# Performance work log

Hardware: AMD Instinct MI355X
Metric: run time of the kernel (lower is better)

## Reference

```python
import jax, jax.numpy as jnp
import numpy as np

N_NODES = 100000
N_EDGES = 1600000
IN_CH = 128
HEADS = 4
HID = 32
OUT_CH = 128
NEG_SLOPE = 0.2


def setup_inputs() -> dict:
    key = jax.random.key(0)
    ks = jax.random.split(key, 7)
    sc = 1.0 / np.sqrt(IN_CH)
    return {
        "x": jax.random.normal(ks[0], (N_NODES, IN_CH), dtype=jnp.float32),
        "edge_index": jax.random.randint(ks[1], (2, N_EDGES), 0, N_NODES, dtype=jnp.int32),
        "W": jax.random.normal(ks[2], (IN_CH, HEADS * HID), dtype=jnp.float32) * sc,
        "att_src": jax.random.normal(ks[3], (HEADS, HID), dtype=jnp.float32) * sc,
        "att_dst": jax.random.normal(ks[4], (HEADS, HID), dtype=jnp.float32) * sc,
        "lin_w": jax.random.normal(ks[5], (HEADS * HID, OUT_CH), dtype=jnp.float32) * (1.0 / np.sqrt(HEADS * HID)),
        "lin_b": jax.random.normal(ks[6], (OUT_CH,), dtype=jnp.float32) * 0.01,
    }


def reference(x, edge_index, W, att_src, att_dst, lin_w, lin_b):
    N = x.shape[0]
    src, dst = edge_index[0], edge_index[1]
    # node-wise linear transform -> [N, H, C]
    h = (x @ W).reshape(N, HEADS, HID)
    # per-node attention logit components [N, H]
    a_src = jnp.einsum("nhc,hc->nh", h, att_src)
    a_dst = jnp.einsum("nhc,hc->nh", h, att_dst)
    # per-edge logits with LeakyReLU [E, H]
    e = jax.nn.leaky_relu(a_src[src] + a_dst[dst], negative_slope=NEG_SLOPE)
    # segment softmax over destination neighborhoods
    m = jax.ops.segment_max(e, dst, num_segments=N)
    ex = jnp.exp(e - m[dst])
    s = jax.ops.segment_sum(ex, dst, num_segments=N)
    alpha = ex / (s[dst] + 1e-16)
    # weighted scatter-sum of source features [N, H, C] -> concat heads
    msg = h[src] * alpha[:, :, None]
    out = jax.ops.segment_sum(msg, dst, num_segments=N).reshape(N, HEADS * HID)
    # trailing dense + ReLU
    return jax.nn.relu(out @ lin_w + lin_b)
```

## Files before the change

### kernel.cpp

```cpp
#include <hip/hip_runtime.h>
#include <hip/hip_fp16.h>

#define NB    256
#define BSH   9
#define HBLK  384
#define BBLK  512

typedef _Float16 f16;
typedef _Float16 half8 __attribute__((ext_vector_type(8)));
typedef __fp16 pk16x2 __attribute__((ext_vector_type(2)));
typedef float f32x4 __attribute__((ext_vector_type(4)));

__global__ __launch_bounds__(256) void k_setup(
    const float* __restrict__ W, const float* __restrict__ LW,
    f16* __restrict__ Wt, f16* __restrict__ LWt,
    const int* __restrict__ dst, int* __restrict__ btot, int E, int chunk)
{
    int b = blockIdx.x;
    int t = threadIdx.x;
    if (b < 128) {
        if (t < 128) Wt[b * 128 + t]           = (f16)W[t * 128 + b];
        else         LWt[b * 128 + (t - 128)]  = (f16)LW[(t - 128) * 128 + b];
        return;
    }
    __shared__ int h[NB];
    h[t] = 0;
    __syncthreads();
    int blk = b - 128;
    int e0 = blk * chunk;
    int e1 = min(e0 + chunk, E);
    for (int e = e0 + t; e < e1; e += 256)
        atomicAdd(&h[dst[e] >> BSH], 1);
    __syncthreads();
    if (h[t]) atomicAdd(&btot[t], h[t]);
}

__global__ __launch_bounds__(256) void k_gemm_att(
    const float* __restrict__ A, const f16* __restrict__ Wt,
    const float* __restrict__ att_s, const float* __restrict__ att_d,
    f16* __restrict__ Hh, float* __restrict__ as_out, float* __restrict__ ad_out,
    int M)
{
    __shared__ __align__(16) f16 as_lds[64 * 136];
    int t = threadIdx.x;
    int row0 = blockIdx.x * 64;

    {
        int r = t >> 2, kq = (t & 3) * 32;
        const float* ap = A + (size_t)(row0 + r) * 128 + kq;
        bool valid = (row0 + r) < M;
        pk16x2 hb[16];
#pragma unroll
        for (int j = 0; j < 8; ++j) {
            float4 v = valid ? *(const float4*)(ap + j * 4) : make_float4(0.f, 0.f, 0.f, 0.f);
            hb[2 * j]     = __builtin_amdgcn_cvt_pkrtz(v.x, v.y);
            hb[2 * j + 1] = __builtin_amdgcn_cvt_pkrtz(v.z, v.w);
        }
        f16* dst = as_lds + r * 136 + kq;
#pragma unroll
        for (int j = 0; j < 4; ++j) *(float4*)(dst + j * 8) = ((float4*)hb)[j];
    }
    __syncthreads();

    int w = t >> 6, ln = t & 63;
    int rr = (w & 1) * 32;
    int cc = (w >> 1) * 64;
    int q = ln >> 4, m = ln & 15;

    f32x4 acc[2][4];
#pragma unroll
    for (int i = 0; i < 2; ++i)
#pragma unroll
        for (int j = 0; j < 4; ++j) acc[i][j] = (f32x4){0.f, 0.f, 0.f, 0.f};

    const f16* wp = Wt + (size_t)(cc + m) * 128 + q * 8;
#pragma unroll
    for (int ks = 0; ks < 4; ++ks) {
        int k0 = ks * 32 + q * 8;
        half8 a0 = *(const half8*)(as_lds + (rr + m) * 136 + k0);
        half8 a1 = *(const half8*)(as_lds + (rr + 16 + m) * 136 + k0);
        half8 bf[4];
#pragma unroll
        for (int j = 0; j < 4; ++j)
            bf[j] = *(const half8*)(wp + j * 16 * 128 + ks * 32);
#pragma unroll
        for (int j = 0; j < 4; ++j) {
            acc[0][j] = __builtin_amdgcn_mfma_f32_16x16x32_f16(a0, bf[j], acc[0][j], 0, 0, 0);
            acc[1][j] = __builtin_amdgcn_mfma_f32_16x16x32_f16(a1, bf[j], acc[1][j], 0, 0, 0);
        }
    }
    __syncthreads();
#pragma unroll
    for (int i = 0; i < 2; ++i)
#pragma unroll
        for (int j = 0; j < 4; ++j)
#pragma unroll
            for (int g = 0; g < 4; ++g)
                as_lds[(rr + i * 16 + q * 4 + g) * 136 + cc + j * 16 + m] = (f16)acc[i][j][g];
    __syncthreads();
    {
        int r = t >> 2, cq = (t & 3) * 32;
        if (row0 + r < M) {
            float4 o0 = *(const float4*)(as_lds + r * 136 + cq);
            float4 o1 = *(const float4*)(as_lds + r * 136 + cq + 8);
            float4 o2 = *(const float4*)(as_lds + r * 136 + cq + 16);
            float4 o3 = *(const float4*)(as_lds + r * 136 + cq + 24);
            float4* hp = (float4*)(Hh + (size_t)(row0 + r) * 128 + cq);
            hp[0] = o0; hp[1] = o1; hp[2] = o2; hp[3] = o3;
        }
    }
    {
        int rl = w * 16 + m;
        int head = q;
        float ds = 0.f, dd = 0.f;
#pragma unroll
        for (int ch = 0; ch < 4; ++ch) {
            half8 hv = *(const half8*)(as_lds + rl * 136 + head * 32 + ch * 8);
            float4 s0 = *(const float4*)(att_s + head * 32 + ch * 8);
            float4 s1 = *(const float4*)(att_s + head * 32 + ch * 8 + 4);
            float4 d0 = *(const float4*)(att_d + head * 32 + ch * 8);
            float4 d1 = *(const float4*)(att_d + head * 32 + ch * 8 + 4);
            ds += (float)hv[0] * s0.x + (float)hv[1] * s0.y + (float)hv[2] * s0.z + (float)hv[3] * s0.w
                + (float)hv[4] * s1.x + (float)hv[5] * s1.y + (float)hv[6] * s1.z + (float)hv[7] * s1.w;
            dd += (float)hv[0] * d0.x + (float)hv[1] * d0.y + (float)hv[2] * d0.z + (float)hv[3] * d0.w
                + (float)hv[4] * d1.x + (float)hv[5] * d1.y + (float)hv[6] * d1.z + (float)hv[7] * d1.w;
        }
        if (row0 + rl < M) {
            as_out[(row0 + rl) * 4 + head] = ds;
            ad_out[(row0 + rl) * 4 + head] = dd;
        }
    }
}

__global__ __launch_bounds__(256) void k_bin(
    const int* __restrict__ ei, const int* __restrict__ btot,
    int* __restrict__ bres, int* __restrict__ binned, int E, int chunk)
{
    __shared__ int h[NB];
    __shared__ int base_s[NB];
    __shared__ int ws[4];
    int t = threadIdx.x;
    {
        int v = btot[t];
        int lane = t & 63, w = t >> 6;
        int x = v;
#pragma unroll
        for (int o = 1; o < 64; o <<= 1) {
            int y = __shfl_up(x, o);
            if (lane >= o) x += y;
        }
        if (lane == 63) ws[w] = x;
        __syncthreads();
        int wb = 0;
#pragma unroll
        for (int k = 0; k < 4; ++k) wb += (k < w) ? ws[k] : 0;
        base_s[t] = wb + x - v;
    }
    h[t] = 0;
    __syncthreads();
    int e0 = blockIdx.x * chunk;
    int e1 = min(e0 + chunk, E);
    for (int e = e0 + t; e < e1; e += 256)
        atomicAdd(&h[ei[E + e] >> BSH], 1);
    __syncthreads();
    int cnt = h[t];
    int mybase = base_s[t] + (cnt ? atomicAdd(&bres[t], cnt) : 0);
    __syncthreads();
    h[t] = mybase;
    __syncthreads();
    for (int e = e0 + t; e < e1; e += 256) {
        int s = ei[e];
        int d = ei[E + e];
        int p = atomicAdd(&h[d >> BSH], 1);
        binned[p] = s | ((d & ((1 << BSH) - 1)) << 17);
    }
}

__global__ __launch_bounds__(256) void k_ph_csr(
    const int* __restrict__ binned, const int* __restrict__ btot,
    int* __restrict__ csr, int* __restrict__ off, int* __restrict__ deg,
    int N, int E)
{
    __shared__ int cnt[512], loff[512], sd[256];
    __shared__ int base_s[NB];
    __shared__ int ws[4];
    int b = blockIdx.x;
    int lo = b << BSH;
    if (lo >= N) return;
    int t = threadIdx.x;
    {
        int v = btot[t];
        int lane = t & 63, w = t >> 6;
        int x = v;
#pragma unroll
        for (int o = 1; o < 64; o <<= 1) {
            int y = __shfl_up(x, o);
            if (lane >= o) x += y;
        }
        if (lane == 63) ws[w] = x;
        __syncthreads();
        int wb = 0;
#pragma unroll
        for (int k = 0; k < 4; ++k) wb += (k < w) ? ws[k] : 0;
        base_s[t] = wb + x - v;
    }
    cnt[t] = 0; cnt[t + 256] = 0;
    __syncthreads();
    int seg = base_s[b];
    int len = btot[b];
    for (int i = t; i < len; i += 256)
        atomicAdd(&cnt[(unsigned)binned[seg + i] >> 17], 1);
    __syncthreads();
    int a0 = cnt[2 * t], a1 = cnt[2 * t + 1];
    int s = a0 + a1;
    sd[t] = s;
    __syncthreads();
    for (int o = 1; o < 256; o <<= 1) {
        int x = (t >= o) ? sd[t - o] : 0;
        __syncthreads();
        sd[t] += x;
        __syncthreads();
    }
    int ex = sd[t] - s;
    loff[2 * t] = ex;
    loff[2 * t + 1] = ex + a0;
    int n0 = lo + 2 * t;
    if (n0 < N)     { off[n0] = seg + ex;          deg[n0] = a0; }
    if (n0 + 1 < N) { off[n0 + 1] = seg + ex + a0; deg[n0 + 1] = a1; }
    __syncthreads();
    for (int i = t; i < len; i += 256) {
        int v = binned[seg + i];
        int p = atomicAdd(&loff[(unsigned)v >> 17], 1);
        csr[seg + p] = v & 0x1ffff;
    }
}

__global__ __launch_bounds__(256) void k_gather_fused(
    const __half* __restrict__ Hh, const float* __restrict__ as_,
    const float* __restrict__ ad_, const int* __restrict__ off,
    const int* __restrict__ deg, const int* __restrict__ csr,
    const f16* __restrict__ LWt, const float* __restrict__ bias,
    float* __restrict__ Out, int N)
{
    __shared__ __align__(16) __half2 wh[16][68];
    __shared__ int srcs[16][16];
    __shared__ __align__(16) f16 pt[16][136];
    int t = threadIdx.x;
    int wid = t >> 6, lane = t & 63;
    int sub = lane >> 4;
    int li = lane & 15;
    int hh = li >> 2;
    int slot = wid * 4 + sub;
    int gbase = blockIdx.x * 16;
    int n = gbase + slot;
    bool nvalid = n < N;
    int dg = nvalid ? deg[n] : 0;
    int base = nvalid ? off[n] : 0;
    float4 adn = nvalid ? *(const float4*)(ad_ + (size_t)n * 4)
                        : make_float4(0.f, 0.f, 0.f, 0.f);

    float s0 = 0.f, s1 = 0.f, s2 = 0.f, s3 = 0.f;
    float acc[8] = {0.f, 0.f, 0.f, 0.f, 0.f, 0.f, 0.f, 0.f};

    for (int c0 = 0; c0 < dg; c0 += 16) {
        int cnt = min(16, dg - c0);
        {
            int idx = c0 + li;
            int se = csr[base + min(idx, dg - 1)];
            float4 as = *(const float4*)(as_ + (size_t)se * 4);
            float e0 = as.x + adn.x, e1 = as.y + adn.y;
            float e2 = as.z + adn.z, e3 = as.w + adn.w;
            e0 = fmaxf(e0, 0.2f * e0); e1 = fmaxf(e1, 0.2f * e1);
            e2 = fmaxf(e2, 0.2f * e2); e3 = fmaxf(e3, 0.2f * e3);
            float x0 = __expf(e0), x1 = __expf(e1);
            float x2 = __expf(e2), x3 = __expf(e3);
            if (idx >= dg) { x0 = x1 = x2 = x3 = 0.f; }
            s0 += x0; s1 += x1; s2 += x2; s3 += x3;
            __half2 w4[4];
            w4[0] = __float2half2_rn(x0);
            w4[1] = __float2half2_rn(x1);
            w4[2] = __float2half2_rn(x2);
            w4[3] = __float2half2_rn(x3);
            *(float4*)&wh[slot][li * 4] = *(float4*)w4;
            srcs[slot][li] = se;
        }
        __asm__ volatile("s_waitcnt lgkmcnt(0)" ::: "memory");
        int quads = (cnt + 3) >> 2;
        __half2 ah[4];
        ah[0] = ah[1] = ah[2] = ah[3] = __float2half2_rn(0.f);
        for (int qq = 0; qq < quads; ++qq) {
#pragma unroll
            for (int u = 0; u < 4; ++u) {
                int i = qq * 4 + u;
                __half2 w2 = wh[slot][i * 4 + hh];
                int se = srcs[slot][i];
                float4 raw = *(const float4*)(Hh + (size_t)se * 128 + li * 8);
                __half2* ph = (__half2*)&raw;
                ah[0] = __hfma2(ph[0], w2, ah[0]);
                ah[1] = __hfma2(ph[1], w2, ah[1]);
                ah[2] = __hfma2(ph[2], w2, ah[2]);
                ah[3] = __hfma2(ph[3], w2, ah[3]);
            }
            if ((qq & 1) == 1) {
#pragma unroll
                for (int k = 0; k < 4; ++k) {
                    float2 f = __half22float2(ah[k]);
                    acc[2 * k] += f.x; acc[2 * k + 1] += f.y;
                    ah[k] = __float2half2_rn(0.f);
                }
            }
        }
#pragma unroll
        for (int k = 0; k < 4; ++k) {
            float2 f = __half22float2(ah[k]);
            acc[2 * k] += f.x; acc[2 * k + 1] += f.y;
        }
        __asm__ volatile("s_waitcnt lgkmcnt(0)" ::: "memory");
    }

#pragma unroll
    for (int o = 1; o < 16; o <<= 1) {
        s0 += __shfl_xor(s0, o);
        s1 += __shfl_xor(s1, o);
        s2 += __shfl_xor(s2, o);
        s3 += __shfl_xor(s3, o);
    }
    float sh = (hh == 0) ? s0 : (hh == 1) ? s1 : (hh == 2) ? s2 : s3;
    float inv = 1.f / (sh + 1e-16f);
    {
        __half2 o4[4];
#pragma unroll
        for (int k = 0; k < 4; ++k)
            o4[k] = __float22half2_rn(make_float2(acc[2 * k] * inv, acc[2 * k + 1] * inv));
        *(float4*)&pt[slot][li * 8] = *(float4*)o4;
    }
    __syncthreads();

    {
        int cc = wid * 32;
        f32x4 acc2[2];
        acc2[0] = (f32x4){0.f, 0.f, 0.f, 0.f};
        acc2[1] = (f32x4){0.f, 0.f, 0.f, 0.f};
        const f16* wp = LWt + (size_t)(cc + li) * 128 + sub * 8;
#pragma unroll
        for (int ks = 0; ks < 4; ++ks) {
            half8 a0 = *(const half8*)&pt[li][ks * 32 + sub * 8];
            half8 b0 = *(const half8*)(wp + ks * 32);
            half8 b1 = *(const half8*)(wp + 16 * 128 + ks * 32);
            acc2[0] = __builtin_amdgcn_mfma_f32_16x16x32_f16(a0, b0, acc2[0], 0, 0, 0);
            acc2[1] = __builtin_amdgcn_mfma_f32_16x16x32_f16(a0, b1, acc2[1], 0, 0, 0);
        }
        float bv0 = bias[cc + li];
        float bv1 = bias[cc + 16 + li];
#pragma unroll
        for (int g = 0; g < 4; ++g) {
            int r = sub * 4 + g;
            int node = gbase + r;
            if (node < N) {
                Out[(size_t)node * 128 + cc + li]      = fmaxf(acc2[0][g] + bv0, 0.f);
                Out[(size_t)node * 128 + cc + 16 + li] = fmaxf(acc2[1][g] + bv1, 0.f);
            }
        }
    }
}


extern "C" void kernel_launch(void* const* d_in, const int* in_sizes, int n_in,
                              void* d_out, int out_size, void* d_ws, size_t ws_size,
                              hipStream_t stream)
{
    const float* x     = (const float*)d_in[0];
    const int*   ei    = (const int*)d_in[1];
    const float* W     = (const float*)d_in[2];
    const float* att_s = (const float*)d_in[3];
    const float* att_d = (const float*)d_in[4];
    const float* lin_w = (const float*)d_in[5];
    const float* lin_b = (const float*)d_in[6];
    float* out = (float*)d_out;
    int N = in_sizes[0] / 128;
    int E = in_sizes[1] / 2;

    char* p = (char*)d_ws;
    auto alloc = [&](size_t bytes) { char* r = p; p += (bytes + 255) & ~(size_t)255; return r; };
    f16*    Hh   = (f16*)alloc((size_t)N * 128 * 2);
    f16*    Wt   = (f16*)alloc(128 * 128 * 2);
    f16*    LWt  = (f16*)alloc(128 * 128 * 2);
    float*  AS   = (float*)alloc((size_t)N * 4 * 4);
    float*  AD   = (float*)alloc((size_t)N * 4 * 4);
    int*    deg  = (int*)alloc((size_t)N * 4);
    int*    off  = (int*)alloc((size_t)N * 4);
    int*    btot = (int*)alloc((size_t)NB * 4 * 2);
    int*    bres = btot + NB;
    int*    csr  = (int*)alloc((size_t)E * 4);
    int*    binned = (int*)alloc((size_t)E * 4);

    int hchunk = (E + HBLK - 1) / HBLK;
    int bchunk = (E + BBLK - 1) / BBLK;
    int mb = (N + 63) / 64;
    hipMemsetAsync(btot, 0, (size_t)NB * 4 * 2, stream);
    k_setup<<<128 + HBLK, 256, 0, stream>>>(W, lin_w, Wt, LWt, ei + E, btot, E, hchunk);
    k_gemm_att<<<mb, 256, 0, stream>>>(x, Wt, att_s, att_d, Hh, AS, AD, N);
    k_bin<<<BBLK, 256, 0, stream>>>(ei, btot, bres, binned, E, bchunk);
    k_ph_csr<<<NB, 256, 0, stream>>>(binned, btot, csr, off, deg, N, E);
    k_gather_fused<<<(N + 15) / 16, 256, 0, stream>>>(
        (const __half*)Hh, AS, AD, off, deg, csr, LWt, lin_b, out, N);
}
```

Baseline: 280.5 us.

## Double-buffer gather feature loads and halve CSR bin width

The gather loop now loads the next quad of source feature rows into a second register buffer while the current quad is accumulated, so global load latency overlaps with the half-precision FMAs. Separately, destination bins shrink from 512 to 256 nodes, giving 512 bins. The per-block full prefix scan in the CSR kernel is replaced by a reduction over the preceding bin totals. The cost is more registers for the double buffer and extra redundant loads at the tail, since indices are clamped to quad 0.

```diff
diff --git a/kernel.cpp b/kernel.cpp
--- a/kernel.cpp
+++ b/kernel.cpp
@@ -1,8 +1,8 @@
 #include <hip/hip_runtime.h>
 #include <hip/hip_fp16.h>
 
-#define NB    256
-#define BSH   9
+#define NB    512
+#define BSH   8
 #define HBLK  384
 #define BBLK  512
 
@@ -24,7 +24,7 @@
         return;
     }
     __shared__ int h[NB];
-    h[t] = 0;
+    h[t] = 0; h[t + 256] = 0;
     __syncthreads();
     int blk = b - 128;
     int e0 = blk * chunk;
@@ -32,7 +32,8 @@
     for (int e = e0 + t; e < e1; e += 256)
         atomicAdd(&h[dst[e] >> BSH], 1);
     __syncthreads();
-    if (h[t]) atomicAdd(&btot[t], h[t]);
+    if (h[t])       atomicAdd(&btot[t], h[t]);
+    if (h[t + 256]) atomicAdd(&btot[t + 256], h[t + 256]);
 }
 
 __global__ __launch_bounds__(256) void k_gemm_att(
@@ -141,9 +142,10 @@
     __shared__ int ws[4];
     int t = threadIdx.x;
     {
-        int v = btot[t];
+        int v0 = btot[2 * t], v1 = btot[2 * t + 1];
+        int s = v0 + v1;
         int lane = t & 63, w = t >> 6;
-        int x = v;
+        int x = s;
 #pragma unroll
         for (int o = 1; o < 64; o <<= 1) {
             int y = __shfl_up(x, o);
@@ -154,19 +156,22 @@
         int wb = 0;
 #pragma unroll
         for (int k = 0; k < 4; ++k) wb += (k < w) ? ws[k] : 0;
-        base_s[t] = wb + x - v;
-    }
-    h[t] = 0;
+        int ex = wb + x - s;
+        base_s[2 * t] = ex;
+        base_s[2 * t + 1] = ex + v0;
+    }
+    h[t] = 0; h[t + 256] = 0;
     __syncthreads();
     int e0 = blockIdx.x * chunk;
     int e1 = min(e0 + chunk, E);
     for (int e = e0 + t; e < e1; e += 256)
         atomicAdd(&h[ei[E + e] >> BSH], 1);
     __syncthreads();
-    int cnt = h[t];
-    int mybase = base_s[t] + (cnt ? atomicAdd(&bres[t], cnt) : 0);
-    __syncthreads();
-    h[t] = mybase;
+    int c0 = h[t], c1 = h[t + 256];
+    int b0 = base_s[t]       + (c0 ? atomicAdd(&bres[t], c0) : 0);
+    int b1 = base_s[t + 256] + (c1 ? atomicAdd(&bres[t + 256], c1) : 0);
+    __syncthreads();
+    h[t] = b0; h[t + 256] = b1;
     __syncthreads();
     for (int e = e0 + t; e < e1; e += 256) {
         int s = ei[e];
@@ -181,39 +186,27 @@
     int* __restrict__ csr, int* __restrict__ off, int* __restrict__ deg,
     int N, int E)
 {
-    __shared__ int cnt[512], loff[512], sd[256];
-    __shared__ int base_s[NB];
+    __shared__ int cnt[256], loff[256], sd[256];
     __shared__ int ws[4];
     int b = blockIdx.x;
     int lo = b << BSH;
     if (lo >= N) return;
     int t = threadIdx.x;
-    {
-        int v = btot[t];
-        int lane = t & 63, w = t >> 6;
-        int x = v;
-#pragma unroll
-        for (int o = 1; o < 64; o <<= 1) {
-            int y = __shfl_up(x, o);
-            if (lane >= o) x += y;
-        }
-        if (lane == 63) ws[w] = x;
-        __syncthreads();
-        int wb = 0;
-#pragma unroll
-        for (int k = 0; k < 4; ++k) wb += (k < w) ? ws[k] : 0;
-        base_s[t] = wb + x - v;
-    }
-    cnt[t] = 0; cnt[t + 256] = 0;
-    __syncthreads();
-    int seg = base_s[b];
+    int lane = t & 63, w = t >> 6;
+    int partial = 0;
+    for (int i = t; i < b; i += 256) partial += btot[i];
+#pragma unroll
+    for (int o = 1; o < 64; o <<= 1) partial += __shfl_xor(partial, o);
+    if (lane == 0) ws[w] = partial;
+    cnt[t] = 0;
+    __syncthreads();
+    int seg = ws[0] + ws[1] + ws[2] + ws[3];
     int len = btot[b];
     for (int i = t; i < len; i += 256)
         atomicAdd(&cnt[(unsigned)binned[seg + i] >> 17], 1);
     __syncthreads();
-    int a0 = cnt[2 * t], a1 = cnt[2 * t + 1];
-    int s = a0 + a1;
-    sd[t] = s;
+    int a = cnt[t];
+    sd[t] = a;
     __syncthreads();
     for (int o = 1; o < 256; o <<= 1) {
         int x = (t >= o) ? sd[t - o] : 0;
@@ -221,12 +214,10 @@
         sd[t] += x;
         __syncthreads();
     }
-    int ex = sd[t] - s;
-    loff[2 * t] = ex;
-    loff[2 * t + 1] = ex + a0;
-    int n0 = lo + 2 * t;
-    if (n0 < N)     { off[n0] = seg + ex;          deg[n0] = a0; }
-    if (n0 + 1 < N) { off[n0 + 1] = seg + ex + a0; deg[n0 + 1] = a1; }
+    int ex = sd[t] - a;
+    loff[t] = ex;
+    int n0 = lo + t;
+    if (n0 < N) { off[n0] = seg + ex; deg[n0] = a; }
     __syncthreads();
     for (int i = t; i < len; i += 256) {
         int v = binned[seg + i];
@@ -288,32 +279,51 @@
         int quads = (cnt + 3) >> 2;
         __half2 ah[4];
         ah[0] = ah[1] = ah[2] = ah[3] = __float2half2_rn(0.f);
-        for (int qq = 0; qq < quads; ++qq) {
+        float4 buf0[4], buf1[4];
+#pragma unroll
+        for (int u = 0; u < 4; ++u) {
+            int se = srcs[slot][u];
+            buf0[u] = *(const float4*)(Hh + (size_t)se * 128 + li * 8);
+        }
+        for (int qq = 0; qq < quads; qq += 2) {
+            int nq1 = (qq + 1 < quads) ? (qq + 1) : 0;
 #pragma unroll
             for (int u = 0; u < 4; ++u) {
-                int i = qq * 4 + u;
-                __half2 w2 = wh[slot][i * 4 + hh];
-                int se = srcs[slot][i];
-                float4 raw = *(const float4*)(Hh + (size_t)se * 128 + li * 8);
-                __half2* ph = (__half2*)&raw;
+                int se = srcs[slot][nq1 * 4 + u];
+                buf1[u] = *(const float4*)(Hh + (size_t)se * 128 + li * 8);
+            }
+#pragma unroll
+            for (int u = 0; u < 4; ++u) {
+                __half2 w2 = wh[slot][(qq * 4 + u) * 4 + hh];
+                __half2* ph = (__half2*)&buf0[u];
                 ah[0] = __hfma2(ph[0], w2, ah[0]);
                 ah[1] = __hfma2(ph[1], w2, ah[1]);
                 ah[2] = __hfma2(ph[2], w2, ah[2]);
                 ah[3] = __hfma2(ph[3], w2, ah[3]);
             }
-            if ((qq & 1) == 1) {
-#pragma unroll
-                for (int k = 0; k < 4; ++k) {
-                    float2 f = __half22float2(ah[k]);
-                    acc[2 * k] += f.x; acc[2 * k + 1] += f.y;
-                    ah[k] = __float2half2_rn(0.f);
+            int nq2 = (qq + 2 < quads) ? (qq + 2) : 0;
+#pragma unroll
+            for (int u = 0; u < 4; ++u) {
+                int se = srcs[slot][nq2 * 4 + u];
+                buf0[u] = *(const float4*)(Hh + (size_t)se * 128 + li * 8);
+            }
+            if (qq + 1 < quads) {
+#pragma unroll
+                for (int u = 0; u < 4; ++u) {
+                    __half2 w2 = wh[slot][((qq + 1) * 4 + u) * 4 + hh];
+                    __half2* ph = (__half2*)&buf1[u];
+                    ah[0] = __hfma2(ph[0], w2, ah[0]);
+                    ah[1] = __hfma2(ph[1], w2, ah[1]);
+                    ah[2] = __hfma2(ph[2], w2, ah[2]);
+                    ah[3] = __hfma2(ph[3], w2, ah[3]);
                 }
             }
-        }
-#pragma unroll
-        for (int k = 0; k < 4; ++k) {
-            float2 f = __half22float2(ah[k]);
-            acc[2 * k] += f.x; acc[2 * k + 1] += f.y;
+#pragma unroll
+            for (int k = 0; k < 4; ++k) {
+                float2 f = __half22float2(ah[k]);
+                acc[2 * k] += f.x; acc[2 * k + 1] += f.y;
+                ah[k] = __float2half2_rn(0.f);
+            }
         }
         __asm__ volatile("s_waitcnt lgkmcnt(0)" ::: "memory");
     }
```

Result: no change. 285.2 us (+1.7%).
